# Performance work log

Measured on AMD Instinct MI355X. Metric: run time of the kernel, lower is better.

Reference implementation:

```python
import jax, jax.numpy as jnp
import numpy as np

N, D, H, DPE, WALK, L, E = 2048, 512, 8, 16, 8, 3, 32768
HD = D // H
DFF = 4 * D


def setup_inputs() -> dict:
    key = jax.random.key(0)
    ks = jax.random.split(key, 16)
    s = 0.02
    return {
        "node_features": jax.random.normal(ks[0], (N, D), jnp.float32),
        "edge_index": jax.random.randint(ks[1], (2, E), 0, N, dtype=jnp.int32),
        "pe_proj_W": jax.random.normal(ks[2], (WALK, DPE), jnp.float32) * s,
        "pe_proj_b": jnp.zeros((DPE,), jnp.float32),
        "qkv_W": jax.random.normal(ks[3], (L, D, 3 * D), jnp.float32) * s,
        "qkv_b": jnp.zeros((L, 3 * D), jnp.float32),
        "peb_W": jax.random.normal(ks[4], (L, DPE, H), jnp.float32) * s,
        "peb_b": jnp.zeros((L, H), jnp.float32),
        "out_W": jax.random.normal(ks[5], (L, D, D), jnp.float32) * s,
        "out_b": jnp.zeros((L, D), jnp.float32),
        "ffn_W1": jax.random.normal(ks[6], (L, D, DFF), jnp.float32) * s,
        "ffn_b1": jnp.zeros((L, DFF), jnp.float32),
        "ffn_W2": jax.random.normal(ks[7], (L, DFF, D), jnp.float32) * s,
        "ffn_b2": jnp.zeros((L, D), jnp.float32),
        "ln1_g": jnp.ones((L, D), jnp.float32),
        "ln1_b": jnp.zeros((L, D), jnp.float32),
        "ln2_g": jnp.ones((L, D), jnp.float32),
        "ln2_b": jnp.zeros((L, D), jnp.float32),
    }


def _layer_norm(x, g, b, eps=1e-5):
    mu = x.mean(-1, keepdims=True)
    var = ((x - mu) ** 2).mean(-1, keepdims=True)
    return (x - mu) * jax.lax.rsqrt(var + eps) * g + b


def _rw_pe(edge_index, pe_proj_W, pe_proj_b, dtype):
    src, tgt = edge_index[0], edge_index[1]
    adj = jnp.zeros((N, N), dtype).at[src, tgt].set(1.0).at[tgt, src].set(1.0)
    deg = jnp.maximum(adj.sum(axis=1, keepdims=True), 1.0)
    T = adj / deg  # row-stochastic transition matrix

    def step(Tk, _):
        return Tk @ T, jnp.diagonal(Tk)

    _, diags = jax.lax.scan(step, T, None, length=WALK)  # [WALK, N]
    rw = diags.T  # [N, WALK] k-step return probabilities
    return rw @ pe_proj_W + pe_proj_b  # [N, DPE]


def reference(node_features, edge_index, pe_proj_W, pe_proj_b, qkv_W, qkv_b,
              peb_W, peb_b, out_W, out_b, ffn_W1, ffn_b1, ffn_W2, ffn_b2,
              ln1_g, ln1_b, ln2_g, ln2_b):
    pe = _rw_pe(edge_index, pe_proj_W, pe_proj_b, node_features.dtype)
    scale = HD ** -0.5
    x = node_features
    for l in range(L):
        qkv = (x @ qkv_W[l] + qkv_b[l]).reshape(N, 3, H, HD)
        q = jnp.transpose(qkv[:, 0], (1, 0, 2))  # [H, N, HD]
        k = jnp.transpose(qkv[:, 1], (1, 0, 2))
        v = jnp.transpose(qkv[:, 2], (1, 0, 2))
        pe_p = pe @ peb_W[l] + peb_b[l]  # [N, H]
        # bias[h, i, j] = pe_p[i, h] - pe_p[j, h]
        bias = pe_p.T[:, :, None] - pe_p.T[:, None, :]
        scores = jnp.einsum('hnd,hmd->hnm', q, k) * scale + bias
        attn = jax.nn.softmax(scores, axis=-1)
        o = jnp.einsum('hnm,hmd->hnd', attn, v)
        o = jnp.transpose(o, (1, 0, 2)).reshape(N, D) @ out_W[l] + out_b[l]
        x = _layer_norm(x + o, ln1_g[l], ln1_b[l])
        h = jax.nn.gelu(x @ ffn_W1[l] + ffn_b1[l], approximate=False)
        h = h @ ffn_W2[l] + ffn_b2[l]
        x = _layer_norm(x + h, ln2_g[l], ln2_b[l])
    return x
```

## Files before the change

kernel.cpp:

```cpp
#include <hip/hip_runtime.h>
#include <cstdint>
#include <cstddef>

#define NN 2048
#define DM 512
#define NH 8
#define HD 64
#define NL 3
#define NE 32768

typedef unsigned short u16;
typedef unsigned int u32;
typedef __attribute__((ext_vector_type(8))) short short8;
typedef __attribute__((ext_vector_type(4))) float float4v;

__device__ __forceinline__ float bf2f(u16 s){
  union { unsigned u; float f; } v; v.u = ((unsigned)s) << 16; return v.f;
}
__device__ __forceinline__ u16 f2bf(float f){
  union { float f; unsigned u; } v; v.f = f;
  unsigned r = v.u + 0x7fffu + ((v.u >> 16) & 1u);
  return (u16)(r >> 16);
}
__device__ __forceinline__ u16 f2bf_fast(float f){
  union { float f; unsigned u; } v; v.f = f;
  return (u16)((v.u + 0x8000u) >> 16);
}
__device__ __forceinline__ void gl_lds16(const void* g, void* l){
  __builtin_amdgcn_global_load_lds((const __attribute__((address_space(1))) void*)g,
                                   (__attribute__((address_space(3))) void*)l, 16, 0, 0);
}

__global__ void adj_scatter(const int* __restrict__ ei, float* __restrict__ A){
  int e = blockIdx.x*256 + threadIdx.x;
  if (e < NE){
    int s = ei[e], t = ei[NE + e];
    A[(size_t)s*NN + t] = 1.f;
    A[(size_t)t*NN + s] = 1.f;
  }
}

__global__ __launch_bounds__(256)
void rowsum_dinv(const float* __restrict__ A, float* __restrict__ dinv){
  int row = blockIdx.x, tid = threadIdx.x;
  __shared__ float red[4];
  float s = 0.f;
  for (int j=tid;j<NN;j+=256) s += A[(size_t)row*NN + j];
  #pragma unroll
  for (int off=32;off>0;off>>=1) s += __shfl_down(s, off);
  if ((tid&63)==0) red[tid>>6] = s;
  __syncthreads();
  if (tid==0) dinv[row] = rsqrtf(fmaxf(red[0]+red[1]+red[2]+red[3], 1.f));
}

__global__ __launch_bounds__(256)
void build_s_nz(const float* __restrict__ A, const float* __restrict__ dinv,
                u16* __restrict__ S, u32* __restrict__ nz, int* __restrict__ cnt){
  const int i = blockIdx.x, tid = threadIdx.x;
  __shared__ int lc;
  if (tid==0) lc = 0;
  __syncthreads();
  const float di = dinv[i];
  for (int j=tid; j<NN; j+=256){
    float a = A[(size_t)i*NN + j];
    u16 v = f2bf(a * di * dinv[j]);
    S[(size_t)i*NN + j] = v;
    if (v){
      int s = atomicAdd(&lc, 1);
      if (s < 128) nz[i*128 + s] = ((u32)j << 16) | v;
    }
  }
  __syncthreads();
  if (tid==0) cnt[i] = lc < 128 ? lc : 128;
}

__global__ __launch_bounds__(256)
void spmm_sq(const u32* __restrict__ nz, const int* __restrict__ cnt,
             u16* __restrict__ S2)
{
  const int j = blockIdx.x, tid = threadIdx.x;
  __shared__ float row[2048];
  __shared__ u32 lnz[128];
  __shared__ int lcnt;
  for (int c=tid;c<2048;c+=256) row[c] = 0.f;
  if (tid==0) lcnt = cnt[j];
  if (tid<128) lnz[tid] = nz[j*128 + tid];
  __syncthreads();
  const int n = lcnt;
  const int g = tid >> 3, sub = tid & 7;
  for (int e = g; e < n; e += 32){
    u32 p = lnz[e];
    int k = p >> 16;
    float wv = bf2f((u16)(p & 0xffffu));
    int m = cnt[k];
    for (int f = sub; f < m; f += 8){
      u32 qq = nz[k*128 + f];
      atomicAdd(&row[qq >> 16], wv * bf2f((u16)(qq & 0xffffu)));
    }
  }
  __syncthreads();
  short8 o;
  #pragma unroll
  for (int t=0;t<8;t++) o[t] = (short)f2bf(row[tid*8 + t]);
  *(short8*)&S2[(size_t)j*NN + tid*8] = o;
}

__global__ __launch_bounds__(256)
void spmm(const u16* __restrict__ Bold, const u32* __restrict__ nz,
          const int* __restrict__ cnt, u16* __restrict__ Bnew)
{
  const int j = blockIdx.x, tid = threadIdx.x;
  __shared__ u32 lnz[128];
  __shared__ int lcnt;
  if (tid==0) lcnt = cnt[j];
  if (tid<128) lnz[tid] = nz[j*128 + tid];
  __syncthreads();
  const int n = lcnt;
  float acc[8] = {0,0,0,0,0,0,0,0};
  for (int e=0; e<n; e++){
    u32 p = lnz[e];
    int k = p >> 16;
    float wv = bf2f((u16)(p & 0xffffu));
    short8 rv = *(const short8*)&Bold[(size_t)k*NN + tid*8];
    #pragma unroll
    for (int t=0;t<8;t++) acc[t] = fmaf(bf2f((u16)rv[t]), wv, acc[t]);
  }
  short8 o;
  #pragma unroll
  for (int t=0;t<8;t++) o[t] = (short)f2bf(acc[t]);
  *(short8*)&Bnew[(size_t)j*NN + tid*8] = o;
}

__global__ __launch_bounds__(256)
void diag_pe(const u16* __restrict__ S, const u16* __restrict__ S2,
             const u16* __restrict__ S3, const u16* __restrict__ S4,
             const float* __restrict__ peW, const float* __restrict__ peb,
             const float* __restrict__ pebW, const float* __restrict__ pebb,
             float* __restrict__ pebT)
{
  const int i = blockIdx.x, tid = threadIdx.x;
  float d[7] = {0,0,0,0,0,0,0};
  for (int j=tid;j<NN;j+=256){
    float s1 = bf2f(S [(size_t)i*NN + j]);
    float s2 = bf2f(S2[(size_t)i*NN + j]);
    float s3 = bf2f(S3[(size_t)i*NN + j]);
    float s4 = bf2f(S4[(size_t)i*NN + j]);
    d[0] += s1*s1; d[1] += s1*s2; d[2] += s2*s2; d[3] += s2*s3;
    d[4] += s3*s3; d[5] += s3*s4; d[6] += s4*s4;
  }
  __shared__ float red[28];
  __shared__ float pv[16];
  #pragma unroll
  for (int t=0;t<7;t++){
    float v = d[t];
    #pragma unroll
    for (int off=32;off>0;off>>=1) v += __shfl_down(v, off);
    if ((tid&63)==0) red[t*4 + (tid>>6)] = v;
  }
  __syncthreads();
  if (tid < 16){
    float rr[8];
    rr[0] = bf2f(S[(size_t)i*NN + i]);
    #pragma unroll
    for (int t=0;t<7;t++) rr[t+1] = red[t*4]+red[t*4+1]+red[t*4+2]+red[t*4+3];
    float a = peb[tid];
    #pragma unroll
    for (int k=0;k<8;k++) a += rr[k]*peW[k*16 + tid];
    pv[tid] = a;
  }
  __syncthreads();
  if (tid < 24){
    int l = tid >> 3, h = tid & 7;
    float a = pebb[l*NH + h];
    #pragma unroll
    for (int p=0;p<16;p++) a += pv[p]*pebW[(l*16+p)*NH + h];
    pebT[((size_t)l*NH + h)*NN + i] = a;
  }
}

__global__ void init_x(const float* __restrict__ nf, float* __restrict__ x, u16* __restrict__ xbf){
  size_t i = (size_t)blockIdx.x*256 + threadIdx.x;
  float v = nf[i]; x[i] = v; xbf[i] = f2bf(v);
}

__global__ __launch_bounds__(256)
void transpose_all(const float* __restrict__ qkvW, const float* __restrict__ outW,
                   const float* __restrict__ f1W,  const float* __restrict__ f2W,
                   u16* __restrict__ qkvT, u16* __restrict__ outT,
                   u16* __restrict__ f1T,  u16* __restrict__ f2T)
{
  __shared__ float t[32][33];
  int gid = blockIdx.x;
  int l = gid / 3072, r = gid % 3072;
  const float* W; u16* WT; int K, N, bx, by;
  if (r < 768)      { W=qkvW; WT=qkvT; K=512;  N=1536; bx=r%48;        by=r/48; }
  else if (r < 1024){ int u=r-768;  W=outW; WT=outT; K=512;  N=512;  bx=u%16; by=u/16; }
  else if (r < 2048){ int u=r-1024; W=f1W;  WT=f1T;  K=512;  N=2048; bx=u%64; by=u/64; }
  else              { int u=r-2048; W=f2W;  WT=f2T;  K=2048; N=512;  bx=u%16; by=u/16; }
  W  += (size_t)l*K*N;
  WT += (size_t)l*K*N;
  int n0 = bx*32, k0 = by*32;
  int tx = threadIdx.x & 31, ty = threadIdx.x >> 5;
  #pragma unroll
  for (int i=0;i<32;i+=8) t[ty+i][tx] = W[(size_t)(k0+ty+i)*N + n0+tx];
  __syncthreads();
  #pragma unroll
  for (int i=0;i<32;i+=8) WT[(size_t)(n0+ty+i)*K + k0+tx] = f2bf(t[tx][ty+i]);
}

__global__ __launch_bounds__(256)
void ln_kernel(const float* __restrict__ xin, const float* __restrict__ add, int nsl,
               const float* __restrict__ g, const float* __restrict__ b,
               float* __restrict__ xout, u16* __restrict__ xbf)
{
  const int row = blockIdx.x, tid = threadIdx.x;
  __shared__ float red[8];
  const size_t base = (size_t)row*DM;
  float v0 = xin[base+tid];
  float v1 = xin[base+256+tid];
  for (int s=0;s<nsl;s++){
    v0 += add[(size_t)s*NN*DM + base+tid];
    v1 += add[(size_t)s*NN*DM + base+256+tid];
  }
  float s = v0+v1, sq = v0*v0 + v1*v1;
  #pragma unroll
  for (int off=32; off>0; off>>=1){ s += __shfl_down(s, off); sq += __shfl_down(sq, off); }
  if ((tid&63)==0){ red[tid>>6] = s; red[4+(tid>>6)] = sq; }
  __syncthreads();
  float mean = (red[0]+red[1]+red[2]+red[3]) * (1.f/512.f);
  float var  = (red[4]+red[5]+red[6]+red[7]) * (1.f/512.f) - mean*mean;
  float rstd = rsqrtf(var + 1e-5f);
  float y0 = (v0-mean)*rstd*g[tid]     + b[tid];
  float y1 = (v1-mean)*rstd*g[256+tid] + b[256+tid];
  xout[base+tid] = y0;     xout[base+256+tid] = y1;
  xbf[base+tid]  = f2bf(y0); xbf[base+256+tid] = f2bf(y1);
}

template<int OUTMODE, int GELU, int BIAS, int ACOMB>
__device__ __forceinline__ void gemm32_body(
    u16* As, u16* Bs, float* invLs,
    const u16* __restrict__ A, const u16* __restrict__ BT,
    const float* __restrict__ bias, void* __restrict__ Cout,
    const u16* __restrict__ Opart, const float* __restrict__ Lsum,
    int M, int N, int K, int ldc, int kper, int bm, int bn, int bz)
{
  const int tid = threadIdx.x, lane = tid & 63, wave = tid >> 6;
  const int q = lane >> 4, lo = lane & 15;
  const int wm = wave >> 1, wn = wave & 1;
  const int k_begin = bz * kper;
  const int kiters = kper >> 6;
  const int srow   = lane >> 3;
  const int gchunk = (lane & 7) ^ srow;

  const u16* Bg = BT + ((size_t)bn*64 + 16*wave + srow) * (size_t)K + k_begin + gchunk*8;
  const size_t r8 = (size_t)8 * K;
  const int Bwoff = wave * 1024;

  const u16* Ag = nullptr;
  const int Awoff = wave * 512;
  if (!ACOMB)
    Ag = A + ((size_t)bm*32 + wave*8 + srow) * (size_t)K + k_begin + gchunk*8;

  int c_sr=0, c_gc=0, c_qb=0, c_rr=0;
  if (ACOMB){
    c_sr = tid >> 3; c_gc = tid & 7;
    c_qb = bm >> 2; c_rr = (bm & 3)*32 + c_sr;
    int hh = tid & 7, rr2 = (bm & 3)*32 + (tid >> 3);
    float L = 0.f;
    #pragma unroll
    for (int ks=0;ks<4;ks++)
      L += Lsum[(((ks*NH + hh)*16 + c_qb))*128 + rr2];
    invLs[(tid>>3)*8 + hh] = 1.f / L;
    __syncthreads();
  }

  float4v acc[2] = {};

  if (ACOMB){
    const int h0 = bz * kiters;
    float a8[8] = {0,0,0,0,0,0,0,0};
    #pragma unroll
    for (int ks=0;ks<4;ks++){
      short8 p = *(const short8*)&Opart[((size_t)((ks*NH + h0)*16 + c_qb))*8192 + c_rr*64 + c_gc*8];
      #pragma unroll
      for (int t=0;t<8;t++) a8[t] += bf2f((u16)p[t]);
    }
    float il = invLs[c_sr*8 + h0 - bz*kiters*0];
    il = invLs[c_sr*8 + (h0 & 7)];
    short8 o;
    #pragma unroll
    for (int t=0;t<8;t++) o[t] = (short)f2bf_fast(a8[t]*il);
    *(short8*)&As[c_sr*64 + ((c_gc ^ (c_sr&7))*8)] = o;
  } else {
    gl_lds16(Ag, As + Awoff);
  }
  gl_lds16(Bg,      Bs + Bwoff);
  gl_lds16(Bg + r8, Bs + Bwoff + 512);

  for (int it = 0; it < kiters; ++it){
    const int curA = (it & 1) << 11, nxtA = curA ^ 2048;
    const int curB = (it & 1) << 12, nxtB = curB ^ 4096;
    __syncthreads();
    if (it + 1 < kiters){
      const int ko = (it+1)*64;
      if (ACOMB){
        const int h = bz*kiters + it + 1;
        float a8[8] = {0,0,0,0,0,0,0,0};
        #pragma unroll
        for (int ks=0;ks<4;ks++){
          short8 p = *(const short8*)&Opart[((size_t)((ks*NH + h)*16 + c_qb))*8192 + c_rr*64 + c_gc*8];
          #pragma unroll
          for (int t=0;t<8;t++) a8[t] += bf2f((u16)p[t]);
        }
        float il = invLs[c_sr*8 + (h & 7)];
        short8 o;
        #pragma unroll
        for (int t=0;t<8;t++) o[t] = (short)f2bf_fast(a8[t]*il);
        *(short8*)&As[nxtA + c_sr*64 + ((c_gc ^ (c_sr&7))*8)] = o;
      } else {
        gl_lds16(Ag + ko, As + nxtA + Awoff);
      }
      gl_lds16(Bg + ko,      Bs + nxtB + Bwoff);
      gl_lds16(Bg + ko + r8, Bs + nxtB + Bwoff + 512);
    }
    const short8* Ar = (const short8*)(As + curA);
    const short8* Br = (const short8*)(Bs + curB);
    #pragma unroll
    for (int kk=0;kk<2;kk++){
      const int cx = (kk*4 + q) ^ (lo & 7);
      short8 af = Ar[(16*wm + lo)*8 + cx];
      #pragma unroll
      for (int nt=0;nt<2;nt++){
        short8 bfr = Br[(32*wn + 16*nt + lo)*8 + cx];
        acc[nt] = __builtin_amdgcn_mfma_f32_16x16x32_bf16(af, bfr, acc[nt], 0, 0, 0);
      }
    }
  }

  float* Cf = (float*)Cout;
  u16*   Cb = (u16*)Cout;
  const size_t zoff = (OUTMODE == 2) ? (size_t)bz * M * ldc : 0;
  const int row = bm*32 + 16*wm + q*4;
  #pragma unroll
  for (int nt=0;nt<2;nt++){
    const int col = bn*64 + 32*wn + 16*nt + lo;
    float bbc = (BIAS==1) ? bias[col] : 0.f;
    #pragma unroll
    for (int r=0;r<4;r++){
      float v = acc[nt][r];
      float bb = (BIAS==2) ? bias[row+r] : bbc;
      if (OUTMODE == 2){
        if (BIAS && bz == 0) v += bb;
        Cf[zoff + (size_t)(row+r)*ldc + col] = v;
      } else {
        v += bb;
        if (GELU) v = 0.5f*v*(1.f + erff(v*0.70710678118654752f));
        if (OUTMODE == 1) Cb[(size_t)(row+r)*ldc + col] = f2bf(v);
        else              Cf[(size_t)(row+r)*ldc + col] = v;
      }
    }
  }
}

template<int OUTMODE, int GELU, int BIAS>
__global__ __launch_bounds__(256)
void gemm32(const u16* __restrict__ A, const u16* __restrict__ BT,
            const float* __restrict__ bias, void* __restrict__ Cout,
            int M, int N, int K, int ldc, int kper)
{
  __shared__ u16 As[2*2048];
  __shared__ u16 Bs[2*4096];
  __shared__ float invLs[256];
  gemm32_body<OUTMODE,GELU,BIAS,0>(As, Bs, invLs, A, BT, bias, Cout, nullptr, nullptr,
                                   M, N, K, ldc, kper, blockIdx.y, blockIdx.x, blockIdx.z);
}

__global__ __launch_bounds__(256)
void qkvt_fused(const u16* __restrict__ xbf, const u16* __restrict__ qkT,
                const float* __restrict__ qkb, u16* __restrict__ qkB,
                const u16* __restrict__ vwT, const float* __restrict__ vb,
                u16* __restrict__ vT)
{
  __shared__ u16 As[2*2048];
  __shared__ u16 Bs[2*4096];
  __shared__ float invLs[256];
  int id = blockIdx.x;
  if (id < 1024)
    gemm32_body<1,0,1,0>(As, Bs, invLs, xbf, qkT, qkb, qkB, nullptr, nullptr,
                         2048, 1024, 512, 1024, 512, id >> 4, id & 15, 0);
  else {
    id -= 1024;
    gemm32_body<1,0,2,0>(As, Bs, invLs, vwT, xbf, vb, vT, nullptr, nullptr,
                         512, 2048, 512, 2048, 512, id >> 5, id & 31, 0);
  }
}

__global__ __launch_bounds__(256)
void outproj_comb(const u16* __restrict__ Opart, const float* __restrict__ Lsum,
                  const u16* __restrict__ outT, const float* __restrict__ outb,
                  float* __restrict__ Cslices)
{
  __shared__ u16 As[2*2048];
  __shared__ u16 Bs[2*4096];
  __shared__ float invLs[256];
  gemm32_body<2,0,1,1>(As, Bs, invLs, nullptr, outT, outb, Cslices, Opart, Lsum,
                       2048, 512, 512, 512, 256, blockIdx.y, blockIdx.x, blockIdx.z);
}

__global__ __launch_bounds__(256)
void attn_part(const u16* __restrict__ qkB, const u16* __restrict__ vT,
               const float* __restrict__ pebT, u16* __restrict__ Opart,
               float* __restrict__ Lsum)
{
  __shared__ u16 Ks[2][64*72];
  __shared__ u16 Vs[2][64*72];
  __shared__ u16 Ps[128*72];
  __shared__ float CB[2][64];
  const int tid = threadIdx.x, lane = tid&63, wave = tid>>6;
  const int q = lane>>4, lo = lane&15;
  const int qb = blockIdx.x, h = blockIdx.y, ks = blockIdx.z;
  const int i0 = qb*128;
  const int part = (ks*NH + h)*16 + qb;

  short8 qf[2][2];
  #pragma unroll
  for (int mt=0;mt<2;mt++)
    #pragma unroll
    for (int kk=0;kk<2;kk++)
      qf[kk][mt] = *(const short8*)&qkB[(size_t)(i0 + 32*wave + 16*mt + lo)*1024 + h*64 + kk*32 + q*8];

  float l_r[2][4] = {};
  float4v o_acc[2][4] = {};

  const int srow = tid >> 2, soff = (tid & 3) * 16;
  const int j_begin = ks*512, j_end = j_begin + 512;

  {
    float4v k0a = *(const float4v*)&qkB[(size_t)(j_begin+srow)*1024 + 512 + h*64 + soff];
    float4v k0b = *(const float4v*)&qkB[(size_t)(j_begin+srow)*1024 + 512 + h*64 + soff + 8];
    float4v v0a = *(const float4v*)&vT[(size_t)(h*64+srow)*NN + j_begin + soff];
    float4v v0b = *(const float4v*)&vT[(size_t)(h*64+srow)*NN + j_begin + soff + 8];
    *(float4v*)&Ks[0][srow*72 + soff]     = k0a;
    *(float4v*)&Ks[0][srow*72 + soff + 8] = k0b;
    *(float4v*)&Vs[0][srow*72 + soff]     = v0a;
    *(float4v*)&Vs[0][srow*72 + soff + 8] = v0b;
    if (tid < 64) CB[0][tid] = pebT[(size_t)h*NN + j_begin + tid] * 1.4426950408889634f;
  }
  __syncthreads();

  for (int j0 = j_begin; j0 < j_end; j0 += 64){
    const int cur = ((j0 - j_begin) >> 6) & 1, nxt = cur ^ 1;
    const bool has_next = (j0 + 64 < j_end);
    float4v ka, kb, va, vb; float cbr = 0.f;
    if (has_next){
      ka = *(const float4v*)&qkB[(size_t)(j0+64+srow)*1024 + 512 + h*64 + soff];
      kb = *(const float4v*)&qkB[(size_t)(j0+64+srow)*1024 + 512 + h*64 + soff + 8];
      va = *(const float4v*)&vT[(size_t)(h*64+srow)*NN + j0+64 + soff];
      vb = *(const float4v*)&vT[(size_t)(h*64+srow)*NN + j0+64 + soff + 8];
      if (tid < 64) cbr = pebT[(size_t)h*NN + j0+64 + tid] * 1.4426950408889634f;
    }

    float4v sacc[2][4] = {};
    const short8* Kr = (const short8*)Ks[cur];
    #pragma unroll
    for (int kk=0; kk<2; kk++){
      #pragma unroll
      for (int nt=0; nt<4; nt++){
        short8 bfr = Kr[(16*nt + lo)*9 + kk*4 + q];
        #pragma unroll
        for (int mt=0; mt<2; mt++)
          sacc[mt][nt] = __builtin_amdgcn_mfma_f32_16x16x32_bf16(qf[kk][mt], bfr, sacc[mt][nt], 0,0,0);
      }
    }
    #pragma unroll
    for (int mt=0; mt<2; mt++)
      #pragma unroll
      for (int nt=0; nt<4; nt++){
        float cb = CB[cur][16*nt + lo];
        #pragma unroll
        for (int r=0;r<4;r++){
          float p = exp2f(fmaf(sacc[mt][nt][r], 0.180336880f, -cb));
          l_r[mt][r] += p;
          Ps[(32*wave + 16*mt + q*4 + r)*72 + 16*nt + lo] = f2bf_fast(p);
        }
      }
    const short8* Pr = (const short8*)Ps;
    const short8* Vr = (const short8*)Vs[cur];
    #pragma unroll
    for (int kk=0;kk<2;kk++){
      #pragma unroll
      for (int mt=0;mt<2;mt++){
        short8 af = Pr[(32*wave + 16*mt + lo)*9 + kk*4 + q];
        #pragma unroll
        for (int nt=0;nt<4;nt++){
          short8 bfr = Vr[(16*nt + lo)*9 + kk*4 + q];
          o_acc[mt][nt] = __builtin_amdgcn_mfma_f32_16x16x32_bf16(af, bfr, o_acc[mt][nt], 0,0,0);
        }
      }
    }
    if (has_next){
      *(float4v*)&Ks[nxt][srow*72 + soff]     = ka;
      *(float4v*)&Ks[nxt][srow*72 + soff + 8] = kb;
      *(float4v*)&Vs[nxt][srow*72 + soff]     = va;
      *(float4v*)&Vs[nxt][srow*72 + soff + 8] = vb;
      if (tid < 64) CB[nxt][tid] = cbr;
    }
    __syncthreads();
  }

  u16* Op = Opart + (size_t)part*8192;
  #pragma unroll
  for (int mt=0;mt<2;mt++){
    #pragma unroll
    for (int r=0;r<4;r++){
      float s = l_r[mt][r];
      s += __shfl_xor(s, 1);
      s += __shfl_xor(s, 2);
      s += __shfl_xor(s, 4);
      s += __shfl_xor(s, 8);
      if (lo == 0) Lsum[part*128 + 32*wave + 16*mt + q*4 + r] = s;
    }
    #pragma unroll
    for (int nt=0;nt<4;nt++)
      #pragma unroll
      for (int r=0;r<4;r++)
        Op[(32*wave + 16*mt + q*4 + r)*64 + 16*nt + lo] = f2bf_fast(o_acc[mt][nt][r]);
  }
}

extern "C" void kernel_launch(void* const* d_in, const int* in_sizes, int n_in,
                              void* d_out, int out_size, void* d_ws, size_t ws_size,
                              hipStream_t stream) {
  const float* nf   = (const float*)d_in[0];
  const int*   ei   = (const int*)d_in[1];
  const float* peW  = (const float*)d_in[2];
  const float* peb  = (const float*)d_in[3];
  const float* qkvW = (const float*)d_in[4];
  const float* qkvb = (const float*)d_in[5];
  const float* pebW = (const float*)d_in[6];
  const float* pebb = (const float*)d_in[7];
  const float* outW = (const float*)d_in[8];
  const float* outb = (const float*)d_in[9];
  const float* f1W  = (const float*)d_in[10];
  const float* f1b  = (const float*)d_in[11];
  const float* f2W  = (const float*)d_in[12];
  const float* f2b  = (const float*)d_in[13];
  const float* ln1g = (const float*)d_in[14];
  const float* ln1b = (const float*)d_in[15];
  const float* ln2g = (const float*)d_in[16];
  const float* ln2b = (const float*)d_in[17];
  (void)in_sizes; (void)n_in; (void)out_size; (void)ws_size;

  char* w = (char*)d_ws;
  constexpr size_t OFF_A     = 0;
  constexpr size_t OFF_S     = OFF_A + 16777216;
  constexpr size_t OFF_S2    = OFF_S + 8388608;
  constexpr size_t OFF_S3    = OFF_S2 + 8388608;
  constexpr size_t OFF_S4    = OFF_S3 + 8388608;
  constexpr size_t OFF_DINV  = OFF_S4 + 8388608;
  constexpr size_t OFF_PEBT  = OFF_DINV + 8192;
  constexpr size_t OFF_QKVT  = OFF_PEBT + 196608;
  constexpr size_t OFF_OUTT  = OFF_QKVT + 4718592;
  constexpr size_t OFF_F1T   = OFF_OUTT + 1572864;
  constexpr size_t OFF_F2T   = OFF_F1T + 6291456;
  constexpr size_t OFF_X     = OFF_F2T + 6291456;
  constexpr size_t OFF_XBF   = OFF_X + 4194304;
  constexpr size_t OFF_QKB   = OFF_XBF + 2097152;
  constexpr size_t OFF_VT    = OFF_QKB + 4194304;
  constexpr size_t OFF_NZ    = OFF_VT + 2097152;
  constexpr size_t OFF_CNT   = OFF_NZ + 1048576;
  constexpr size_t OFF_LS    = OFF_CNT + 8192;
  constexpr size_t OFF_HBUF  = OFF_LS + 262144;

  float* A     = (float*)(w + OFF_A);
  u16*   S     = (u16*)  (w + OFF_S);
  u16*   S2    = (u16*)  (w + OFF_S2);
  u16*   S3    = (u16*)  (w + OFF_S3);
  u16*   S4    = (u16*)  (w + OFF_S4);
  float* dinv  = (float*)(w + OFF_DINV);
  float* pebT  = (float*)(w + OFF_PEBT);
  u16*   qkvT  = (u16*)  (w + OFF_QKVT);
  u16*   outT  = (u16*)  (w + OFF_OUTT);
  u16*   f1T   = (u16*)  (w + OFF_F1T);
  u16*   f2T   = (u16*)  (w + OFF_F2T);
  float* x     = (float*)(w + OFF_X);
  u16*   xbf   = (u16*)  (w + OFF_XBF);
  u16*   qkB   = (u16*)  (w + OFF_QKB);
  u16*   vT    = (u16*)  (w + OFF_VT);
  u32*   NZ    = (u32*)  (w + OFF_NZ);
  int*   CNT   = (int*)  (w + OFF_CNT);
  float* Lsum  = (float*)(w + OFF_LS);
  u16*   hbuf  = (u16*)  (w + OFF_HBUF);
  u16*   Opart   = (u16*)A;
  float* Oslices = (float*)(w + OFF_A + 8388608);
  float* Fslices = (float*)A;

  hipMemsetAsync(A, 0, 16777216, stream);
  adj_scatter<<<dim3(NE/256), 256, 0, stream>>>(ei, A);
  rowsum_dinv<<<dim3(NN), 256, 0, stream>>>(A, dinv);
  build_s_nz<<<dim3(NN), 256, 0, stream>>>(A, dinv, S, NZ, CNT);
  spmm_sq<<<dim3(NN), 256, 0, stream>>>(NZ, CNT, S2);
  spmm<<<dim3(NN), 256, 0, stream>>>(S2, NZ, CNT, S3);
  spmm<<<dim3(NN), 256, 0, stream>>>(S3, NZ, CNT, S4);
  diag_pe<<<dim3(NN), 256, 0, stream>>>(S, S2, S3, S4, peW, peb, pebW, pebb, pebT);

  transpose_all<<<dim3(9216), 256, 0, stream>>>(qkvW, outW, f1W, f2W, qkvT, outT, f1T, f2T);
  init_x<<<dim3(NN*DM/256), 256, 0, stream>>>(nf, x, xbf);

  for (int l = 0; l < NL; l++){
    qkvt_fused<<<dim3(1536), 256, 0, stream>>>(
        xbf, qkvT + (size_t)l*1536*512, qkvb + l*1536, qkB,
        qkvT + (size_t)l*1536*512 + (size_t)1024*512, qkvb + l*1536 + 1024, vT);
    attn_part<<<dim3(16,8,4), 256, 0, stream>>>(qkB, vT, pebT + (size_t)l*NH*NN, Opart, Lsum);

    outproj_comb<<<dim3(8,64,2), 256, 0, stream>>>(
        Opart, Lsum, outT + (size_t)l*512*512, outb + l*512, Oslices);
    ln_kernel<<<dim3(NN), 256, 0, stream>>>(x, Oslices, 2, ln1g + l*512, ln1b + l*512, x, xbf);

    gemm32<1,1,1><<<dim3(32,64,1), 256, 0, stream>>>(
        xbf, f1T + (size_t)l*2048*512, f1b + l*2048, hbuf, 2048, 2048, 512, 2048, 512);
    gemm32<2,0,1><<<dim3(8,64,2), 256, 0, stream>>>(
        hbuf, f2T + (size_t)l*512*2048, f2b + l*512, Fslices, 2048, 512, 2048, 512, 1024);
    float* xout = (l == NL-1) ? (float*)d_out : x;
    ln_kernel<<<dim3(NN), 256, 0, stream>>>(x, Fslices, 2, ln2g + l*512, ln2b + l*512, xout, xbf);
  }
}
```

Measured before the change: 456.5 us.

## Fuse random-walk diagonal computation into SpMM kernels and merge prep launches

Computes the return-probability diagonals incrementally inside the SpMM kernels using S^a·S^b row dot products. This drops the separate diag_pe pass and the S4 matrix. The S^2 build, weight transposes and input conversion are merged into one launch, and the last SpMM step plus PE projection is merged with the first layer's QKV GEMM. The exact erf GELU is replaced by a tanh-style sigmoid approximation, which reduces accuracy slightly. Together these cut kernel launches and full passes over the dense N×N bf16 matrices.

```diff
diff --git a/kernel.cpp b/kernel.cpp
--- a/kernel.cpp
+++ b/kernel.cpp
@@ -75,43 +75,92 @@
 }
 
 __global__ __launch_bounds__(256)
-void spmm_sq(const u32* __restrict__ nz, const int* __restrict__ cnt,
-             u16* __restrict__ S2)
-{
-  const int j = blockIdx.x, tid = threadIdx.x;
-  __shared__ float row[2048];
-  __shared__ u32 lnz[128];
-  __shared__ int lcnt;
-  for (int c=tid;c<2048;c+=256) row[c] = 0.f;
-  if (tid==0) lcnt = cnt[j];
-  if (tid<128) lnz[tid] = nz[j*128 + tid];
-  __syncthreads();
-  const int n = lcnt;
-  const int g = tid >> 3, sub = tid & 7;
-  for (int e = g; e < n; e += 32){
-    u32 p = lnz[e];
-    int k = p >> 16;
-    float wv = bf2f((u16)(p & 0xffffu));
-    int m = cnt[k];
-    for (int f = sub; f < m; f += 8){
-      u32 qq = nz[k*128 + f];
-      atomicAdd(&row[qq >> 16], wv * bf2f((u16)(qq & 0xffffu)));
-    }
-  }
-  __syncthreads();
-  short8 o;
-  #pragma unroll
-  for (int t=0;t<8;t++) o[t] = (short)f2bf(row[tid*8 + t]);
-  *(short8*)&S2[(size_t)j*NN + tid*8] = o;
-}
-
-__global__ __launch_bounds__(256)
-void spmm(const u16* __restrict__ Bold, const u32* __restrict__ nz,
-          const int* __restrict__ cnt, u16* __restrict__ Bnew)
+void fused_prep(const u32* __restrict__ nz, const int* __restrict__ cnt,
+                const u16* __restrict__ S, u16* __restrict__ S2, float* __restrict__ diagsG,
+                const float* __restrict__ qkvW, const float* __restrict__ outW,
+                const float* __restrict__ f1W,  const float* __restrict__ f2W,
+                u16* __restrict__ qkvT, u16* __restrict__ outT,
+                u16* __restrict__ f1T,  u16* __restrict__ f2T,
+                const float* __restrict__ nf, float* __restrict__ x, u16* __restrict__ xbf)
+{
+  __shared__ __align__(16) char sm[8960];
+  const int bid = blockIdx.x, tid = threadIdx.x;
+  if (bid < 2048){
+    float* row  = (float*)sm;
+    u32*   lnz  = (u32*)(sm + 8192);
+    int*   lcnt = (int*)(sm + 8704);
+    float* rbuf = (float*)(sm + 8708);
+    const int j = bid;
+    for (int c=tid;c<2048;c+=256) row[c] = 0.f;
+    if (tid==0) *lcnt = cnt[j];
+    if (tid<128) lnz[tid] = nz[j*128 + tid];
+    __syncthreads();
+    const int n = *lcnt;
+    const int g = tid >> 3, sub = tid & 7;
+    for (int e = g; e < n; e += 32){
+      u32 p = lnz[e];
+      int k = p >> 16;
+      float wv = bf2f((u16)(p & 0xffffu));
+      int m = cnt[k];
+      for (int f = sub; f < m; f += 8){
+        u32 qq = nz[k*128 + f];
+        atomicAdd(&row[qq >> 16], wv * bf2f((u16)(qq & 0xffffu)));
+      }
+    }
+    __syncthreads();
+    short8 sv = *(const short8*)&S[(size_t)j*NN + tid*8];
+    short8 o; float k2=0.f,k3=0.f,k4=0.f;
+    #pragma unroll
+    for (int t=0;t<8;t++){
+      float s2v = row[tid*8 + t], s1v = bf2f((u16)sv[t]);
+      o[t] = (short)f2bf(s2v);
+      k2 += s1v*s1v; k3 += s1v*s2v; k4 += s2v*s2v;
+    }
+    *(short8*)&S2[(size_t)j*NN + tid*8] = o;
+    #pragma unroll
+    for (int off=32;off>0;off>>=1){
+      k2 += __shfl_down(k2,off); k3 += __shfl_down(k3,off); k4 += __shfl_down(k4,off);
+    }
+    if ((tid&63)==0){ int wv_ = tid>>6; rbuf[wv_]=k2; rbuf[4+wv_]=k3; rbuf[8+wv_]=k4; }
+    __syncthreads();
+    if (tid==0){
+      diagsG[j*8+0] = bf2f(S[(size_t)j*NN + j]);
+      diagsG[j*8+1] = rbuf[0]+rbuf[1]+rbuf[2]+rbuf[3];
+      diagsG[j*8+2] = rbuf[4]+rbuf[5]+rbuf[6]+rbuf[7];
+      diagsG[j*8+3] = rbuf[8]+rbuf[9]+rbuf[10]+rbuf[11];
+    }
+  } else if (bid < 2048 + 9216){
+    float (*t)[33] = (float(*)[33])sm;
+    int gid = bid - 2048;
+    int l = gid / 3072, r = gid % 3072;
+    const float* W; u16* WT; int K, N, bx, by;
+    if (r < 768)      { W=qkvW; WT=qkvT; K=512;  N=1536; bx=r%48;        by=r/48; }
+    else if (r < 1024){ int u=r-768;  W=outW; WT=outT; K=512;  N=512;  bx=u%16; by=u/16; }
+    else if (r < 2048){ int u=r-1024; W=f1W;  WT=f1T;  K=512;  N=2048; bx=u%64; by=u/64; }
+    else              { int u=r-2048; W=f2W;  WT=f2T;  K=2048; N=512;  bx=u%16; by=u/16; }
+    W  += (size_t)l*K*N;
+    WT += (size_t)l*K*N;
+    int n0 = bx*32, k0 = by*32;
+    int tx = tid & 31, ty = tid >> 5;
+    #pragma unroll
+    for (int i=0;i<32;i+=8) t[ty+i][tx] = W[(size_t)(k0+ty+i)*N + n0+tx];
+    __syncthreads();
+    #pragma unroll
+    for (int i=0;i<32;i+=8) WT[(size_t)(n0+ty+i)*K + k0+tx] = f2bf(t[tx][ty+i]);
+  } else {
+    size_t i = (size_t)(bid - 11264)*256 + tid;
+    float v = nf[i]; x[i] = v; xbf[i] = f2bf(v);
+  }
+}
+
+__global__ __launch_bounds__(256)
+void spmm_d34(const u16* __restrict__ S2, const u32* __restrict__ nz,
+              const int* __restrict__ cnt, u16* __restrict__ S3, float* __restrict__ diagsG)
 {
   const int j = blockIdx.x, tid = threadIdx.x;
   __shared__ u32 lnz[128];
   __shared__ int lcnt;
+  __shared__ float rbuf[8];
   if (tid==0) lcnt = cnt[j];
   if (tid<128) lnz[tid] = nz[j*128 + tid];
   __syncthreads();
@@ -121,91 +170,27 @@
     u32 p = lnz[e];
     int k = p >> 16;
     float wv = bf2f((u16)(p & 0xffffu));
-    short8 rv = *(const short8*)&Bold[(size_t)k*NN + tid*8];
+    short8 rv = *(const short8*)&S2[(size_t)k*NN + tid*8];
     #pragma unroll
     for (int t=0;t<8;t++) acc[t] = fmaf(bf2f((u16)rv[t]), wv, acc[t]);
   }
-  short8 o;
+  short8 s2v = *(const short8*)&S2[(size_t)j*NN + tid*8];
+  short8 o; float k5=0.f,k6=0.f;
   #pragma unroll
-  for (int t=0;t<8;t++) o[t] = (short)f2bf(acc[t]);
-  *(short8*)&Bnew[(size_t)j*NN + tid*8] = o;
-}
-
-__global__ __launch_bounds__(256)
-void diag_pe(const u16* __restrict__ S, const u16* __restrict__ S2,
-             const u16* __restrict__ S3, const u16* __restrict__ S4,
-             const float* __restrict__ peW, const float* __restrict__ peb,
-             const float* __restrict__ pebW, const float* __restrict__ pebb,
-             float* __restrict__ pebT)
-{
-  const int i = blockIdx.x, tid = threadIdx.x;
-  float d[7] = {0,0,0,0,0,0,0};
-  for (int j=tid;j<NN;j+=256){
-    float s1 = bf2f(S [(size_t)i*NN + j]);
-    float s2 = bf2f(S2[(size_t)i*NN + j]);
-    float s3 = bf2f(S3[(size_t)i*NN + j]);
-    float s4 = bf2f(S4[(size_t)i*NN + j]);
-    d[0] += s1*s1; d[1] += s1*s2; d[2] += s2*s2; d[3] += s2*s3;
-    d[4] += s3*s3; d[5] += s3*s4; d[6] += s4*s4;
-  }
-  __shared__ float red[28];
-  __shared__ float pv[16];
+  for (int t=0;t<8;t++){
+    float a = acc[t], b = bf2f((u16)s2v[t]);
+    o[t] = (short)f2bf(a);
+    k5 += a*b; k6 += a*a;
+  }
+  *(short8*)&S3[(size_t)j*NN + tid*8] = o;
   #pragma unroll
-  for (int t=0;t<7;t++){
-    float v = d[t];
-    #pragma unroll
-    for (int off=32;off>0;off>>=1) v += __shfl_down(v, off);
-    if ((tid&63)==0) red[t*4 + (tid>>6)] = v;
-  }
+  for (int off=32;off>0;off>>=1){ k5 += __shfl_down(k5,off); k6 += __shfl_down(k6,off); }
+  if ((tid&63)==0){ int w_ = tid>>6; rbuf[w_]=k5; rbuf[4+w_]=k6; }
   __syncthreads();
-  if (tid < 16){
-    float rr[8];
-    rr[0] = bf2f(S[(size_t)i*NN + i]);
-    #pragma unroll
-    for (int t=0;t<7;t++) rr[t+1] = red[t*4]+red[t*4+1]+red[t*4+2]+red[t*4+3];
-    float a = peb[tid];
-    #pragma unroll
-    for (int k=0;k<8;k++) a += rr[k]*peW[k*16 + tid];
-    pv[tid] = a;
-  }
-  __syncthreads();
-  if (tid < 24){
-    int l = tid >> 3, h = tid & 7;
-    float a = pebb[l*NH + h];
-    #pragma unroll
-    for (int p=0;p<16;p++) a += pv[p]*pebW[(l*16+p)*NH + h];
-    pebT[((size_t)l*NH + h)*NN + i] = a;
-  }
-}
-
-__global__ void init_x(const float* __restrict__ nf, float* __restrict__ x, u16* __restrict__ xbf){
-  size_t i = (size_t)blockIdx.x*256 + threadIdx.x;
-  float v = nf[i]; x[i] = v; xbf[i] = f2bf(v);
-}
-
-__global__ __launch_bounds__(256)
-void transpose_all(const float* __restrict__ qkvW, const float* __restrict__ outW,
-                   const float* __restrict__ f1W,  const float* __restrict__ f2W,
-                   u16* __restrict__ qkvT, u16* __restrict__ outT,
-                   u16* __restrict__ f1T,  u16* __restrict__ f2T)
-{
-  __shared__ float t[32][33];
-  int gid = blockIdx.x;
-  int l = gid / 3072, r = gid % 3072;
-  const float* W; u16* WT; int K, N, bx, by;
-  if (r < 768)      { W=qkvW; WT=qkvT; K=512;  N=1536; bx=r%48;        by=r/48; }
-  else if (r < 1024){ int u=r-768;  W=outW; WT=outT; K=512;  N=512;  bx=u%16; by=u/16; }
-  else if (r < 2048){ int u=r-1024; W=f1W;  WT=f1T;  K=512;  N=2048; bx=u%64; by=u/64; }
-  else              { int u=r-2048; W=f2W;  WT=f2T;  K=2048; N=512;  bx=u%16; by=u/16; }
-  W  += (size_t)l*K*N;
-  WT += (size_t)l*K*N;
-  int n0 = bx*32, k0 = by*32;
-  int tx = threadIdx.x & 31, ty = threadIdx.x >> 5;
-  #pragma unroll
-  for (int i=0;i<32;i+=8) t[ty+i][tx] = W[(size_t)(k0+ty+i)*N + n0+tx];
-  __syncthreads();
-  #pragma unroll
-  for (int i=0;i<32;i+=8) WT[(size_t)(n0+ty+i)*K + k0+tx] = f2bf(t[tx][ty+i]);
+  if (tid==0){
+    diagsG[j*8+4] = rbuf[0]+rbuf[1]+rbuf[2]+rbuf[3];
+    diagsG[j*8+5] = rbuf[4]+rbuf[5]+rbuf[6]+rbuf[7];
+  }
 }
 
 __global__ __launch_bounds__(256)
@@ -285,8 +270,7 @@
       #pragma unroll
       for (int t=0;t<8;t++) a8[t] += bf2f((u16)p[t]);
     }
-    float il = invLs[c_sr*8 + h0 - bz*kiters*0];
-    il = invLs[c_sr*8 + (h0 & 7)];
+    float il = invLs[c_sr*8 + (h0 & 7)];
     short8 o;
     #pragma unroll
     for (int t=0;t<8;t++) o[t] = (short)f2bf_fast(a8[t]*il);
@@ -354,7 +338,11 @@
         Cf[zoff + (size_t)(row+r)*ldc + col] = v;
       } else {
         v += bb;
-        if (GELU) v = 0.5f*v*(1.f + erff(v*0.70710678118654752f));
+        if (GELU){
+          float t2 = v*v;
+          float y2 = v*(1.5957691216f + 0.07135481283f*t2);
+          v = v / (1.f + exp2f(-1.4426950408889634f*y2));
+        }
         if (OUTMODE == 1) Cb[(size_t)(row+r)*ldc + col] = f2bf(v);
         else              Cf[(size_t)(row+r)*ldc + col] = v;
       }
@@ -392,6 +380,87 @@
     id -= 1024;
     gemm32_body<1,0,2,0>(As, Bs, invLs, vwT, xbf, vb, vT, nullptr, nullptr,
                          512, 2048, 512, 2048, 512, id >> 5, id & 31, 0);
+  }
+}
+
+__global__ __launch_bounds__(256)
+void fused_pe_qkvt(const u16* __restrict__ S3, const u32* __restrict__ nz,
+                   const int* __restrict__ cnt, const float* __restrict__ diagsG,
+                   const float* __restrict__ peW, const float* __restrict__ peb,
+                   const float* __restrict__ pebW, const float* __restrict__ pebb,
+                   float* __restrict__ pebT,
+                   const u16* __restrict__ xbf, const u16* __restrict__ qkT,
+                   const float* __restrict__ qkb, u16* __restrict__ qkB,
+                   const u16* __restrict__ vwT, const float* __restrict__ vb,
+                   u16* __restrict__ vT)
+{
+  __shared__ __align__(16) char sm[25600];
+  int bid = blockIdx.x;
+  const int tid = threadIdx.x;
+  if (bid < 2048){
+    u32*   lnz  = (u32*)sm;
+    int*   lcnt = (int*)(sm + 512);
+    float* rbuf = (float*)(sm + 516);
+    float* rrs  = (float*)(sm + 548);
+    float* pv   = (float*)(sm + 580);
+    const int j = bid;
+    if (tid==0) *lcnt = cnt[j];
+    if (tid<128) lnz[tid] = nz[j*128 + tid];
+    __syncthreads();
+    const int n = *lcnt;
+    float acc[8] = {0,0,0,0,0,0,0,0};
+    for (int e=0; e<n; e++){
+      u32 p = lnz[e];
+      int k = p >> 16;
+      float wv = bf2f((u16)(p & 0xffffu));
+      short8 rv = *(const short8*)&S3[(size_t)k*NN + tid*8];
+      #pragma unroll
+      for (int t=0;t<8;t++) acc[t] = fmaf(bf2f((u16)rv[t]), wv, acc[t]);
+    }
+    short8 s3v = *(const short8*)&S3[(size_t)j*NN + tid*8];
+    float k7=0.f,k8=0.f;
+    #pragma unroll
+    for (int t=0;t<8;t++){
+      float a = acc[t], b = bf2f((u16)s3v[t]);
+      k7 += a*b; k8 += a*a;
+    }
+    #pragma unroll
+    for (int off=32;off>0;off>>=1){ k7 += __shfl_down(k7,off); k8 += __shfl_down(k8,off); }
+    if ((tid&63)==0){ int w_ = tid>>6; rbuf[w_]=k7; rbuf[4+w_]=k8; }
+    if (tid<6) rrs[tid] = diagsG[j*8 + tid];
+    __syncthreads();
+    if (tid==0){
+      rrs[6] = rbuf[0]+rbuf[1]+rbuf[2]+rbuf[3];
+      rrs[7] = rbuf[4]+rbuf[5]+rbuf[6]+rbuf[7];
+    }
+    __syncthreads();
+    if (tid < 16){
+      float a = peb[tid];
+      #pragma unroll
+      for (int k=0;k<8;k++) a += rrs[k]*peW[k*16 + tid];
+      pv[tid] = a;
+    }
+    __syncthreads();
+    if (tid < 24){
+      int l = tid >> 3, h = tid & 7;
+      float a = pebb[l*NH + h];
+      #pragma unroll
+      for (int p=0;p<16;p++) a += pv[p]*pebW[(l*16+p)*NH + h];
+      pebT[((size_t)l*NH + h)*NN + j] = a;
+    }
+  } else {
+    u16*   As    = (u16*)sm;
+    u16*   Bs    = (u16*)(sm + 8192);
+    float* invLs = (float*)(sm + 24576);
+    int id = bid - 2048;
+    if (id < 1024)
+      gemm32_body<1,0,1,0>(As, Bs, invLs, xbf, qkT, qkb, qkB, nullptr, nullptr,
+                           2048, 1024, 512, 1024, 512, id >> 4, id & 15, 0);
+    else {
+      id -= 1024;
+      gemm32_body<1,0,2,0>(As, Bs, invLs, vwT, xbf, vb, vT, nullptr, nullptr,
+                           512, 2048, 512, 2048, 512, id >> 5, id & 31, 0);
+    }
   }
 }
 
@@ -556,8 +625,8 @@
   constexpr size_t OFF_S     = OFF_A + 16777216;
   constexpr size_t OFF_S2    = OFF_S + 8388608;
   constexpr size_t OFF_S3    = OFF_S2 + 8388608;
-  constexpr size_t OFF_S4    = OFF_S3 + 8388608;
-  constexpr size_t OFF_DINV  = OFF_S4 + 8388608;
+  constexpr size_t OFF_DIAG  = OFF_S3 + 8388608;
+  constexpr size_t OFF_DINV  = OFF_DIAG + 65536;
   constexpr size_t OFF_PEBT  = OFF_DINV + 8192;
   constexpr size_t OFF_QKVT  = OFF_PEBT + 196608;
   constexpr size_t OFF_OUTT  = OFF_QKVT + 4718592;
@@ -576,7 +645,7 @@
   u16*   S     = (u16*)  (w + OFF_S);
   u16*   S2    = (u16*)  (w + OFF_S2);
   u16*   S3    = (u16*)  (w + OFF_S3);
-  u16*   S4    = (u16*)  (w + OFF_S4);
+  float* diagsG= (float*)(w + OFF_DIAG);
   float* dinv  = (float*)(w + OFF_DINV);
   float* pebT  = (float*)(w + OFF_PEBT);
   u16*   qkvT  = (u16*)  (w + OFF_QKVT);
@@ -599,18 +668,19 @@
   adj_scatter<<<dim3(NE/256), 256, 0, stream>>>(ei, A);
   rowsum_dinv<<<dim3(NN), 256, 0, stream>>>(A, dinv);
   build_s_nz<<<dim3(NN), 256, 0, stream>>>(A, dinv, S, NZ, CNT);
-  spmm_sq<<<dim3(NN), 256, 0, stream>>>(NZ, CNT, S2);
-  spmm<<<dim3(NN), 256, 0, stream>>>(S2, NZ, CNT, S3);
-  spmm<<<dim3(NN), 256, 0, stream>>>(S3, NZ, CNT, S4);
-  diag_pe<<<dim3(NN), 256, 0, stream>>>(S, S2, S3, S4, peW, peb, pebW, pebb, pebT);
-
-  transpose_all<<<dim3(9216), 256, 0, stream>>>(qkvW, outW, f1W, f2W, qkvT, outT, f1T, f2T);
-  init_x<<<dim3(NN*DM/256), 256, 0, stream>>>(nf, x, xbf);
+  fused_prep<<<dim3(15360), 256, 0, stream>>>(NZ, CNT, S, S2, diagsG,
+      qkvW, outW, f1W, f2W, qkvT, outT, f1T, f2T, nf, x, xbf);
+  spmm_d34<<<dim3(NN), 256, 0, stream>>>(S2, NZ, CNT, S3, diagsG);
+  fused_pe_qkvt<<<dim3(2048 + 1536), 256, 0, stream>>>(S3, NZ, CNT, diagsG,
+      peW, peb, pebW, pebb, pebT,
+      xbf, qkvT, qkvb, qkB,
+      qkvT + (size_t)1024*512, qkvb + 1024, vT);
 
   for (int l = 0; l < NL; l++){
-    qkvt_fused<<<dim3(1536), 256, 0, stream>>>(
-        xbf, qkvT + (size_t)l*1536*512, qkvb + l*1536, qkB,
-        qkvT + (size_t)l*1536*512 + (size_t)1024*512, qkvb + l*1536 + 1024, vT);
+    if (l > 0)
+      qkvt_fused<<<dim3(1536), 256, 0, stream>>>(
+          xbf, qkvT + (size_t)l*1536*512, qkvb + l*1536, qkB,
+          qkvT + (size_t)l*1536*512 + (size_t)1024*512, qkvb + l*1536 + 1024, vT);
     attn_part<<<dim3(16,8,4), 256, 0, stream>>>(qkB, vT, pebT + (size_t)l*NH*NN, Opart, Lsum);
 
     outproj_comb<<<dim3(8,64,2), 256, 0, stream>>>(
```

Result: faster. 435.7 us (-4.6%).
